# Optimization experiments

Measured on AMD Instinct MI355X. Metric: run time of the kernel, lower is better.

Reference implementation:

```python
import jax, jax.numpy as jnp
import numpy as np

N_INP = 128
N_HID = 512
N_OUT = 256
N_HEADS = 64
N_SM = 4
EPS_GN = 1e-5
TINY = 1e-14


def setup_inputs() -> dict:
    key = jax.random.key(0)
    ks = jax.random.split(key, 8)
    s = 0.05  # small init scale keeps softplus/softmax in a sane range
    f32 = jnp.float32
    return {
        "x": jax.random.normal(ks[0], (N_INP, N_INP), f32),
        "last_out_sm": jax.random.uniform(ks[1], (N_OUT, N_HEADS), f32),
        # grouped-conv weights, stored per-head with conv singleton dims squeezed
        "qw": jax.random.normal(ks[2], (N_HEADS, N_INP), f32) * s,            # Conv2d q
        "w1": jax.random.normal(ks[3], (N_HEADS, N_HID, N_INP), f32) * s,     # Conv1d l1
        "gn1_g": jnp.ones((N_HEADS, N_HID), f32),                             # GroupNorm ln_l1
        "gn1_b": jnp.zeros((N_HEADS, N_HID), f32),
        "w2": jax.random.normal(ks[4], (N_SM, N_HEADS, N_OUT, N_HID), f32) * s,  # Conv1d l2_n
        "gn2_g": jnp.ones((N_SM, N_HEADS, N_OUT), f32),                       # GroupNorm ln_l2_n
        "gn2_b": jnp.zeros((N_SM, N_HEADS, N_OUT), f32),
        "ws": jax.random.normal(ks[5], (N_HEADS, N_OUT, N_OUT), f32) * s,     # Conv1d scalar
        "woo": jax.random.normal(ks[6], (N_HEADS, 2 * N_OUT), f32) * s,       # Conv1d on_off
    }


def _group_norm(z, g, b):
    # normalize over the last (per-head channel) axis, biased variance, then affine
    mu = z.mean(-1, keepdims=True)
    var = z.var(-1, keepdims=True)
    return (z - mu) * jax.lax.rsqrt(var + EPS_GN) * g + b


def reference(x, last_out_sm, qw, w1, gn1_g, gn1_b, w2, gn2_g, gn2_b, ws, woo):
    n_out = last_out_sm.shape[0]
    # q: grouped Conv2d with kernel (1, n_inp) on replicated x -> per-head x @ qw_h
    sub = jnp.einsum("rc,hc->hr", x, qw)                     # (H, n_inp)
    # l1 (grouped 1x1 conv == per-head matmul) + GroupNorm(n_heads groups) + softplus
    h1 = jax.nn.softplus(_group_norm(jnp.einsum("hoi,hi->ho", w1, sub), gn1_g, gn1_b))  # (H, n_hid)
    # l2_n branches: per-head matmul + GroupNorm + softmax over n_out, summed over n_sm
    z = _group_norm(jnp.einsum("shoi,hi->sho", w2, h1), gn2_g, gn2_b)  # (S, H, n_out)
    out_sm = jax.nn.softmax(z, axis=-1).sum(0).T             # (n_out, H)
    # scalar branch: grouped 1x1 conv applied to ones -> row-sum of per-head weight
    scalar = ws.sum(-1).T                                    # (n_out, H)
    # on_off gate: per-head dot of [prod(last_out_sm, dim1), out_sm[:, h]] with woo_h
    last_prod = jnp.prod(last_out_sm, axis=1)                # (n_out,)
    gate_logit = woo[:, :n_out] @ last_prod + jnp.einsum("ho,oh->h", woo[:, n_out:], out_sm)
    on_off = jax.nn.sigmoid(gate_logit)                      # (H,)
    on_off_out_sm = on_off[None, :] * out_sm                 # (n_out, H)
    out_scaled = on_off_out_sm * scalar
    out_scaled = jnp.where(jnp.abs(out_scaled) <= TINY, TINY, out_scaled)
    return (jnp.clip(on_off_out_sm, TINY, None), out_scaled)
```

## Files before the change

### kernel.cpp

```cpp
#include <hip/hip_runtime.h>
#include <math.h>

#define N_INP 128
#define N_HID 512
#define N_OUT 256
#define N_HEADS 64
#define N_SM 4
#define EPS_GN 1e-5f
#define TINY 1e-14f

template <int CTRL>
__device__ __forceinline__ float dpp_add(float v) {
  int x = __builtin_amdgcn_update_dpp(0, __float_as_int(v), CTRL, 0xF, 0xF, true);
  return v + __int_as_float(x);
}
__device__ __forceinline__ float red16(float v) {
  v = dpp_add<0x111>(v);
  v = dpp_add<0x112>(v);
  v = dpp_add<0x114>(v);
  v = dpp_add<0x118>(v);
  return v;
}
__device__ __forceinline__ float red32(float v) {
  v = red16(v);
  v = dpp_add<0x142>(v);
  return v;
}
__device__ __forceinline__ float red64(float v) {
  v = red32(v);
  v = dpp_add<0x143>(v);
  return v;
}

__device__ __forceinline__ float block_sum(float v, float* red) {
  int wave = threadIdx.x >> 6, lane = threadIdx.x & 63;
  int nw = blockDim.x >> 6;
  v = red64(v);
  __syncthreads();
  if (lane == 63) red[wave] = v;
  __syncthreads();
  float s = 0.f;
  for (int i = 0; i < nw; ++i) s += red[i];
  return s;
}

__global__ __launch_bounds__(512) void k_z1(
    const float* __restrict__ x, const float* __restrict__ qw,
    const float* __restrict__ w1, float* __restrict__ z1,
    float* __restrict__ zstat) {
  int blk = blockIdx.x;
  int h = blk >> 2, oq = blk & 3;
  int tid = threadIdx.x, lane = tid & 63;
  int g = lane >> 4, gl = lane & 15;
  int grp = (tid >> 6) * 4 + g;
  __shared__ float sub_s[N_INP];
  __shared__ float2 wred[32];

  const float4* qrow = (const float4*)(qw + (size_t)h * N_INP);
  float4 Q0 = qrow[gl], Q1 = qrow[16 + gl];

#pragma unroll
  for (int j = 0; j < 4; ++j) {
    int r = grp + 32 * j;
    const float4* xr = (const float4*)(x + (size_t)r * N_INP);
    float4 X0 = xr[gl], X1 = xr[16 + gl];
    float p = X0.x * Q0.x + X0.y * Q0.y + X0.z * Q0.z + X0.w * Q0.w +
              X1.x * Q1.x + X1.y * Q1.y + X1.z * Q1.z + X1.w * Q1.w;
    p = red16(p);
    if (gl == 15) sub_s[r] = p;
  }
  __syncthreads();

  const float4* sv = (const float4*)sub_s;
  float4 S0 = sv[gl], S1 = sv[16 + gl];
  const float* w1h = w1 + ((size_t)h * N_HID + (size_t)oq * 128) * N_INP;
  float zs = 0.f, zq = 0.f;
#pragma unroll
  for (int j = 0; j < 4; ++j) {
    int o = grp + 32 * j;
    const float4* wr = (const float4*)(w1h + (size_t)o * N_INP);
    float4 W0 = wr[gl], W1 = wr[16 + gl];
    float p = W0.x * S0.x + W0.y * S0.y + W0.z * S0.z + W0.w * S0.w +
              W1.x * S1.x + W1.y * S1.y + W1.z * S1.z + W1.w * S1.w;
    p = red16(p);
    if (gl == 15) { z1[h * N_HID + oq * 128 + o] = p; zs += p; zq += p * p; }
  }
  if (gl == 15) wred[grp] = make_float2(zs, zq);
  __syncthreads();
  if (tid == 0) {
    float a = 0.f, b = 0.f;
#pragma unroll
    for (int i = 0; i < 32; ++i) { a += wred[i].x; b += wred[i].y; }
    zstat[blk * 2] = a;
    zstat[blk * 2 + 1] = b;
  }
}

__global__ __launch_bounds__(1024) void k_l2(
    const float* __restrict__ z1, const float* __restrict__ zstat,
    const float* __restrict__ g1, const float* __restrict__ b1,
    const float* __restrict__ w2, const float* __restrict__ g2,
    const float* __restrict__ b2, const float* __restrict__ wsc,
    float* __restrict__ part, float* __restrict__ scal) {
  int blk = blockIdx.x;
  int s = blk >> 6, h = blk & 63;
  int tid = threadIdx.x, wave = tid >> 6, lane = tid & 63;
  int g32 = lane >> 5, q = lane & 31;
  int g = lane >> 4, gl = lane & 15;
  __shared__ float h1_s[N_HID];
  __shared__ float z_s[N_OUT];
  __shared__ float2 red2[32];
  __shared__ float red[16];

  const float* w2base = w2 + (size_t)blk * N_OUT * N_HID;
  int row0 = wave * 16 + g32 * 8;

  float4 A[4], B[4];
  {
    const float4* rp = (const float4*)(w2base + (size_t)row0 * N_HID) + q;
#pragma unroll
    for (int c = 0; c < 4; ++c) A[c] = rp[c * 32];
  }

  float zsum = 0.f, zsq = 0.f;
#pragma unroll
  for (int qq = 0; qq < 4; ++qq) {
    zsum += zstat[(h * 4 + qq) * 2];
    zsq  += zstat[(h * 4 + qq) * 2 + 1];
  }
  float mu1 = zsum * (1.f / N_HID);
  float var1 = zsq * (1.f / N_HID) - mu1 * mu1;
  float r1 = rsqrtf(var1 + EPS_GN);
  if (tid < N_HID) {
    float v1 = z1[h * N_HID + tid];
    float zz = (v1 - mu1) * r1 * g1[h * N_HID + tid] + b1[h * N_HID + tid];
    h1_s[tid] = fmaxf(zz, 0.f) + log1pf(expf(-fabsf(zz)));
  }
  __syncthreads();

  float4 H[4];
#pragma unroll
  for (int c = 0; c < 4; ++c) H[c] = ((const float4*)h1_s)[q + c * 32];

  float as = 0.f, aq = 0.f;
#pragma unroll
  for (int r = 0; r < 8; ++r) {
    if (r < 7) {
      const float4* rp =
          (const float4*)(w2base + (size_t)(row0 + r + 1) * N_HID) + q;
#pragma unroll
      for (int c = 0; c < 4; ++c) B[c] = rp[c * 32];
    }
    float p = 0.f;
#pragma unroll
    for (int c = 0; c < 4; ++c)
      p += A[c].x * H[c].x + A[c].y * H[c].y + A[c].z * H[c].z + A[c].w * H[c].w;
    p = red32(p);
    if (q == 31) {
      z_s[row0 + r] = p;
      as += p; aq += p * p;
    }
#pragma unroll
    for (int c = 0; c < 4; ++c) A[c] = B[c];
  }
  if (q == 31) red2[wave * 2 + g32] = make_float2(as, aq);

  {
    int o = s * 64 + wave * 4 + g;
    const float4* wr = (const float4*)(wsc + ((size_t)h * N_OUT + o) * N_OUT) + gl;
    float4 v0 = wr[0], v1 = wr[16], v2 = wr[32], v3 = wr[48];
    float p = v0.x + v0.y + v0.z + v0.w + v1.x + v1.y + v1.z + v1.w +
              v2.x + v2.y + v2.z + v2.w + v3.x + v3.y + v3.z + v3.w;
    p = red16(p);
    if (gl == 15) scal[o * N_HEADS + h] = p;
  }
  __syncthreads();

  float sx = 0.f, sy = 0.f;
#pragma unroll
  for (int i = 0; i < 32; ++i) { sx += red2[i].x; sy += red2[i].y; }
  float mu = sx * (1.f / N_OUT);
  float var = sy * (1.f / N_OUT) - mu * mu;
  float rs = rsqrtf(var + EPS_GN);
  float e = (tid < N_OUT)
                ? expf((z_s[tid] - mu) * rs * g2[(size_t)blk * N_OUT + tid] +
                       b2[(size_t)blk * N_OUT + tid])
                : 0.f;
  float es = block_sum(e, red);
  if (tid < N_OUT) part[(size_t)blk * N_OUT + tid] = e / es;
}

__global__ __launch_bounds__(256) void k_gate_final(
    const float* __restrict__ last, const float* __restrict__ woo,
    const float* __restrict__ part, const float* __restrict__ scal,
    float* __restrict__ out) {
  int h = blockIdx.x;
  int tid = threadIdx.x;
  __shared__ float red[4];

  float osum = 0.f;
#pragma unroll
  for (int ss = 0; ss < 4; ++ss)
    osum += part[(size_t)(ss * 64 + h) * N_OUT + tid];

  const float4* rowL = (const float4*)(last + (size_t)tid * N_HEADS);
  float lp = 1.f;
#pragma unroll
  for (int j = 0; j < 16; ++j) {
    float4 v = rowL[j];
    lp *= v.x * v.y * v.z * v.w;
  }
  float gpart = woo[h * 2 * N_OUT + tid] * lp +
                woo[h * 2 * N_OUT + N_OUT + tid] * osum;
  float logit = block_sum(gpart, red);
  float oo = 1.f / (1.f + expf(-logit));

  float v0 = oo * osum;
  out[tid * N_HEADS + h] = fmaxf(v0, TINY);
  float v1 = v0 * scal[tid * N_HEADS + h];
  out[N_OUT * N_HEADS + tid * N_HEADS + h] = (fabsf(v1) <= TINY) ? TINY : v1;
}

extern "C" void kernel_launch(void* const* d_in, const int* in_sizes, int n_in,
                              void* d_out, int out_size, void* d_ws, size_t ws_size,
                              hipStream_t stream) {
  const float* x    = (const float*)d_in[0];
  const float* last = (const float*)d_in[1];
  const float* qw   = (const float*)d_in[2];
  const float* w1   = (const float*)d_in[3];
  const float* g1   = (const float*)d_in[4];
  const float* b1   = (const float*)d_in[5];
  const float* w2   = (const float*)d_in[6];
  const float* g2   = (const float*)d_in[7];
  const float* b2   = (const float*)d_in[8];
  const float* wsc  = (const float*)d_in[9];
  const float* woo  = (const float*)d_in[10];
  float* out = (float*)d_out;
  float* ws  = (float*)d_ws;

  float* z1    = ws;
  float* zstat = ws + 32768;
  float* part  = ws + 33280;
  float* scal  = ws + 98816;

  hipLaunchKernelGGL(k_z1,        dim3(256), dim3(512),  0, stream,
                     x, qw, w1, z1, zstat);
  hipLaunchKernelGGL(k_l2,        dim3(256), dim3(1024), 0, stream,
                     z1, zstat, g1, b1, w2, g2, b2, wsc, part, scal);
  hipLaunchKernelGGL(k_gate_final,dim3(64),  dim3(256),  0, stream,
                     last, woo, part, scal, out);
}
```

Measured before the change: 241.9 us.

## Fuse three kernels into one cooperative kernel with grid syncs

Merges the z1, l2 and gate/final kernels into one cooperative launch of 256 blocks of 1024 threads, with grid.sync() between stages. The w2 row prefetch is issued at kernel start, so the first large load overlaps the z1 stage. This removes two kernel launch gaps and lets the w2 load start before z1 is done. In exchange it adds grid-wide barrier cost, and on this 256-CU part it relies on every block being co-resident.

```diff
diff --git a/kernel.cpp b/kernel.cpp
--- a/kernel.cpp
+++ b/kernel.cpp
@@ -1,5 +1,8 @@
 #include <hip/hip_runtime.h>
+#include <hip/hip_cooperative_groups.h>
 #include <math.h>
+
+namespace cg = cooperative_groups;
 
 #define N_INP 128
 #define N_HID 512
@@ -44,24 +47,44 @@
   return s;
 }
 
-__global__ __launch_bounds__(512) void k_z1(
-    const float* __restrict__ x, const float* __restrict__ qw,
-    const float* __restrict__ w1, float* __restrict__ z1,
-    float* __restrict__ zstat) {
+__global__ __launch_bounds__(1024) void k_fused(
+    const float* __restrict__ x, const float* __restrict__ last,
+    const float* __restrict__ qw, const float* __restrict__ w1,
+    const float* __restrict__ g1, const float* __restrict__ b1,
+    const float* __restrict__ w2, const float* __restrict__ g2,
+    const float* __restrict__ b2, const float* __restrict__ wsc,
+    const float* __restrict__ woo, float* __restrict__ z1,
+    float* __restrict__ zstat, float* __restrict__ part,
+    float* __restrict__ scal, float* __restrict__ out) {
+  cg::grid_group grid = cg::this_grid();
   int blk = blockIdx.x;
-  int h = blk >> 2, oq = blk & 3;
-  int tid = threadIdx.x, lane = tid & 63;
+  int s = blk >> 6, h = blk & 63;
+  int tid = threadIdx.x, wave = tid >> 6, lane = tid & 63;
+  int g32 = lane >> 5, q = lane & 31;
   int g = lane >> 4, gl = lane & 15;
-  int grp = (tid >> 6) * 4 + g;
+  int grp = wave * 4 + g;
+
   __shared__ float sub_s[N_INP];
-  __shared__ float2 wred[32];
+  __shared__ float h1_s[N_HID];
+  __shared__ float z_s[N_OUT];
+  __shared__ float2 red2[64];
+  __shared__ float red[16];
+
+  const float* w2base = w2 + (size_t)blk * N_OUT * N_HID;
+  int row0 = wave * 16 + g32 * 8;
+
+  float4 A[4], B[4];
+  {
+    const float4* rp = (const float4*)(w2base + (size_t)row0 * N_HID) + q;
+#pragma unroll
+    for (int c = 0; c < 4; ++c) A[c] = rp[c * 32];
+  }
 
   const float4* qrow = (const float4*)(qw + (size_t)h * N_INP);
   float4 Q0 = qrow[gl], Q1 = qrow[16 + gl];
-
-#pragma unroll
-  for (int j = 0; j < 4; ++j) {
-    int r = grp + 32 * j;
+#pragma unroll
+  for (int j = 0; j < 2; ++j) {
+    int r = grp + 64 * j;
     const float4* xr = (const float4*)(x + (size_t)r * N_INP);
     float4 X0 = xr[gl], X1 = xr[16 + gl];
     float p = X0.x * Q0.x + X0.y * Q0.y + X0.z * Q0.z + X0.w * Q0.w +
@@ -71,56 +94,33 @@
   }
   __syncthreads();
 
-  const float4* sv = (const float4*)sub_s;
-  float4 S0 = sv[gl], S1 = sv[16 + gl];
-  const float* w1h = w1 + ((size_t)h * N_HID + (size_t)oq * 128) * N_INP;
-  float zs = 0.f, zq = 0.f;
-#pragma unroll
-  for (int j = 0; j < 4; ++j) {
-    int o = grp + 32 * j;
-    const float4* wr = (const float4*)(w1h + (size_t)o * N_INP);
-    float4 W0 = wr[gl], W1 = wr[16 + gl];
-    float p = W0.x * S0.x + W0.y * S0.y + W0.z * S0.z + W0.w * S0.w +
-              W1.x * S1.x + W1.y * S1.y + W1.z * S1.z + W1.w * S1.w;
-    p = red16(p);
-    if (gl == 15) { z1[h * N_HID + oq * 128 + o] = p; zs += p; zq += p * p; }
-  }
-  if (gl == 15) wred[grp] = make_float2(zs, zq);
+  {
+    const float4* sv = (const float4*)sub_s;
+    float4 S0 = sv[gl], S1 = sv[16 + gl];
+    const float* w1h = w1 + ((size_t)h * N_HID + (size_t)s * 128) * N_INP;
+    float zs = 0.f, zq = 0.f;
+#pragma unroll
+    for (int j = 0; j < 2; ++j) {
+      int o = grp + 64 * j;
+      const float4* wr = (const float4*)(w1h + (size_t)o * N_INP);
+      float4 W0 = wr[gl], W1 = wr[16 + gl];
+      float p = W0.x * S0.x + W0.y * S0.y + W0.z * S0.z + W0.w * S0.w +
+                W1.x * S1.x + W1.y * S1.y + W1.z * S1.z + W1.w * S1.w;
+      p = red16(p);
+      if (gl == 15) { z1[h * N_HID + s * 128 + o] = p; zs += p; zq += p * p; }
+    }
+    if (gl == 15) red2[grp] = make_float2(zs, zq);
+  }
   __syncthreads();
   if (tid == 0) {
     float a = 0.f, b = 0.f;
 #pragma unroll
-    for (int i = 0; i < 32; ++i) { a += wred[i].x; b += wred[i].y; }
-    zstat[blk * 2] = a;
-    zstat[blk * 2 + 1] = b;
-  }
-}
-
-__global__ __launch_bounds__(1024) void k_l2(
-    const float* __restrict__ z1, const float* __restrict__ zstat,
-    const float* __restrict__ g1, const float* __restrict__ b1,
-    const float* __restrict__ w2, const float* __restrict__ g2,
-    const float* __restrict__ b2, const float* __restrict__ wsc,
-    float* __restrict__ part, float* __restrict__ scal) {
-  int blk = blockIdx.x;
-  int s = blk >> 6, h = blk & 63;
-  int tid = threadIdx.x, wave = tid >> 6, lane = tid & 63;
-  int g32 = lane >> 5, q = lane & 31;
-  int g = lane >> 4, gl = lane & 15;
-  __shared__ float h1_s[N_HID];
-  __shared__ float z_s[N_OUT];
-  __shared__ float2 red2[32];
-  __shared__ float red[16];
-
-  const float* w2base = w2 + (size_t)blk * N_OUT * N_HID;
-  int row0 = wave * 16 + g32 * 8;
-
-  float4 A[4], B[4];
-  {
-    const float4* rp = (const float4*)(w2base + (size_t)row0 * N_HID) + q;
-#pragma unroll
-    for (int c = 0; c < 4; ++c) A[c] = rp[c * 32];
-  }
+    for (int i = 0; i < 64; ++i) { a += red2[i].x; b += red2[i].y; }
+    zstat[(h * 4 + s) * 2] = a;
+    zstat[(h * 4 + s) * 2 + 1] = b;
+  }
+
+  grid.sync();
 
   float zsum = 0.f, zsq = 0.f;
 #pragma unroll
@@ -188,37 +188,35 @@
                 : 0.f;
   float es = block_sum(e, red);
   if (tid < N_OUT) part[(size_t)blk * N_OUT + tid] = e / es;
-}
-
-__global__ __launch_bounds__(256) void k_gate_final(
-    const float* __restrict__ last, const float* __restrict__ woo,
-    const float* __restrict__ part, const float* __restrict__ scal,
-    float* __restrict__ out) {
-  int h = blockIdx.x;
-  int tid = threadIdx.x;
-  __shared__ float red[4];
-
-  float osum = 0.f;
-#pragma unroll
-  for (int ss = 0; ss < 4; ++ss)
-    osum += part[(size_t)(ss * 64 + h) * N_OUT + tid];
-
-  const float4* rowL = (const float4*)(last + (size_t)tid * N_HEADS);
-  float lp = 1.f;
-#pragma unroll
-  for (int j = 0; j < 16; ++j) {
-    float4 v = rowL[j];
-    lp *= v.x * v.y * v.z * v.w;
-  }
-  float gpart = woo[h * 2 * N_OUT + tid] * lp +
-                woo[h * 2 * N_OUT + N_OUT + tid] * osum;
-  float logit = block_sum(gpart, red);
-  float oo = 1.f / (1.f + expf(-logit));
-
-  float v0 = oo * osum;
-  out[tid * N_HEADS + h] = fmaxf(v0, TINY);
-  float v1 = v0 * scal[tid * N_HEADS + h];
-  out[N_OUT * N_HEADS + tid * N_HEADS + h] = (fabsf(v1) <= TINY) ? TINY : v1;
+
+  grid.sync();
+
+  if (blk < N_HEADS) {
+    int hh = blk;
+    float osum = 0.f, gpart = 0.f;
+    if (tid < N_OUT) {
+#pragma unroll
+      for (int ss = 0; ss < 4; ++ss)
+        osum += part[(size_t)(ss * 64 + hh) * N_OUT + tid];
+      const float4* rowL = (const float4*)(last + (size_t)tid * N_HEADS);
+      float lp = 1.f;
+#pragma unroll
+      for (int j = 0; j < 16; ++j) {
+        float4 v = rowL[j];
+        lp *= v.x * v.y * v.z * v.w;
+      }
+      gpart = woo[hh * 2 * N_OUT + tid] * lp +
+              woo[hh * 2 * N_OUT + N_OUT + tid] * osum;
+    }
+    float logit = block_sum(gpart, red);
+    float oo = 1.f / (1.f + expf(-logit));
+    if (tid < N_OUT) {
+      float v0 = oo * osum;
+      out[tid * N_HEADS + hh] = fmaxf(v0, TINY);
+      float v1 = v0 * scal[tid * N_HEADS + hh];
+      out[N_OUT * N_HEADS + tid * N_HEADS + hh] = (fabsf(v1) <= TINY) ? TINY : v1;
+    }
+  }
 }
 
 extern "C" void kernel_launch(void* const* d_in, const int* in_sizes, int n_in,
@@ -243,10 +241,10 @@
   float* part  = ws + 33280;
   float* scal  = ws + 98816;
 
-  hipLaunchKernelGGL(k_z1,        dim3(256), dim3(512),  0, stream,
-                     x, qw, w1, z1, zstat);
-  hipLaunchKernelGGL(k_l2,        dim3(256), dim3(1024), 0, stream,
-                     z1, zstat, g1, b1, w2, g2, b2, wsc, part, scal);
-  hipLaunchKernelGGL(k_gate_final,dim3(64),  dim3(256),  0, stream,
-                     last, woo, part, scal, out);
-}
+  void* args[] = {(void*)&x,   (void*)&last, (void*)&qw,  (void*)&w1,
+                  (void*)&g1,  (void*)&b1,   (void*)&w2,  (void*)&g2,
+                  (void*)&b2,  (void*)&wsc,  (void*)&woo, (void*)&z1,
+                  (void*)&zstat, (void*)&part, (void*)&scal, (void*)&out};
+  hipLaunchCooperativeKernel((const void*)k_fused, dim3(256), dim3(1024),
+                             args, 0, stream);
+}
```

New measurement: 315.5 us. 1.3x slower.
